# Optimization experiments

Measured on AMD Instinct MI355X. Metric: run time of the kernel, lower is better.

Reference implementation:

```python
import jax, jax.numpy as jnp
import numpy as np


def _ln(x, g, b, eps=1e-5):
    m = x.mean(-1, keepdims=True)
    v = ((x - m) ** 2).mean(-1, keepdims=True)
    return (x - m) / jnp.sqrt(v + eps) * g + b


def _conv(x, w, b, stride, pad, groups):
    # x: NCHW, w: OIHW (I = in_ch/groups)
    out = jax.lax.conv_general_dilated(
        x, w, (stride, stride), [(pad, pad), (pad, pad)],
        dimension_numbers=('NCHW', 'OIHW', 'NCHW'), feature_group_count=groups)
    return out + b[None, :, None, None]


def _gelu(x):
    return jax.nn.gelu(x, approximate=False)  # torch nn.GELU (exact erf)


def _forward(x, H, W, lpu_w, lpu_b, n1_g, n1_b, conv2d_w, conv2d_b, cn_g, cn_b,
             q_w, sr1_w, sr1_b, an1_g, an1_b, sr2_w, sr2_b, an2_g, an2_b,
             kv1_w, kv2_w, proj_w, proj_b, n2_g, n2_b,
             fc1_w, fc1_b, dw_w, dw_b, fc2_w, fc2_b):
    B, N, C = x.shape
    cd = C // 4          # conv_part_dim = 64
    ad = C - cd          # attn_part_dim = 192
    nh = 8
    hg = nh // 2         # heads per group
    hd = ad // nh        # head_dim = 24
    scale = hd ** -0.5
    # ---- LPU: depthwise 3x3 conv residual ----
    xi = x.transpose(0, 2, 1).reshape(B, C, H, W)
    xi = _conv(xi, lpu_w, lpu_b, 1, 1, C) + xi
    x = xi.reshape(B, C, N).transpose(0, 2, 1)
    # ---- Attention branch (pre-LN) ----
    y = _ln(x, n1_g, n1_b)
    cp, ap = y[..., :cd], y[..., cd:]
    # conv part: dense 3x3 conv (sr_ratio==8 -> kernel 3, pad 1), then LN+GELU in NLC
    cp = cp.reshape(B, H, W, cd).transpose(0, 3, 1, 2)
    cp = _conv(cp, conv2d_w, conv2d_b, 1, 1, 1).reshape(B, cd, N).transpose(0, 2, 1)
    cp = _gelu(_ln(cp, cn_g, cn_b))
    # attn part: dual spatial-reduction KV paths
    q = (ap @ q_w.T).reshape(B, N, nh, hd).transpose(0, 2, 1, 3)  # [B,nh,N,hd]
    x_ = ap.transpose(0, 2, 1).reshape(B, ad, H, W)
    x1 = _conv(x_, sr1_w, sr1_b, 8, 0, ad).reshape(B, ad, -1).transpose(0, 2, 1)  # [B,(H/8)(W/8),ad]
    x1 = _gelu(_ln(x1, an1_g, an1_b))
    x2 = _conv(x_, sr2_w, sr2_b, 4, 0, ad).reshape(B, ad, -1).transpose(0, 2, 1)  # [B,(H/4)(W/4),ad]
    x2 = _gelu(_ln(x2, an2_g, an2_b))
    kv1 = (x1 @ kv1_w.T).reshape(B, -1, 2, hg, hd).transpose(2, 0, 3, 1, 4)  # [2,B,hg,M1,hd]
    kv2 = (x2 @ kv2_w.T).reshape(B, -1, 2, hg, hd).transpose(2, 0, 3, 1, 4)

    def attn(qh, k, v):
        a = jax.nn.softmax(jnp.einsum('bhnd,bhmd->bhnm', qh, k) * scale, axis=-1)
        o = jnp.einsum('bhnm,bhmd->bhnd', a, v)
        return o.transpose(0, 2, 1, 3).reshape(B, N, -1)

    o1 = attn(q[:, :hg], kv1[0], kv1[1])
    o2 = attn(q[:, hg:], kv2[0], kv2[1])
    y = jnp.concatenate([o1, o2, cp], axis=-1) @ proj_w.T + proj_b
    x = x + y
    # ---- MLP with depthwise conv ----
    z = _ln(x, n2_g, n2_b) @ fc1_w.T + fc1_b
    hidc = z.shape[-1]
    z = z.transpose(0, 2, 1).reshape(B, hidc, H, W)
    z = _conv(z, dw_w, dw_b, 1, 1, hidc).reshape(B, hidc, N).transpose(0, 2, 1)
    z = _gelu(z) @ fc2_w.T + fc2_b
    return x + z


def setup_inputs() -> dict:
    key = jax.random.key(0)
    ks = jax.random.split(key, 16)
    B, H, W, C = 16, 56, 56, 256
    N = H * W
    cd, ad = C // 4, C * 3 // 4
    hid = 4 * C
    f = lambda i, shape, s=0.02: jax.random.normal(ks[i], shape, jnp.float32) * s
    return dict(
        x=jax.random.normal(ks[0], (B, N, C), jnp.float32),
        H=H, W=W,
        lpu_w=f(1, (C, 1, 3, 3), 0.1), lpu_b=jnp.zeros((C,), jnp.float32),
        n1_g=jnp.ones((C,), jnp.float32), n1_b=jnp.zeros((C,), jnp.float32),
        conv2d_w=f(2, (cd, cd, 3, 3), 0.05), conv2d_b=jnp.zeros((cd,), jnp.float32),
        cn_g=jnp.ones((cd,), jnp.float32), cn_b=jnp.zeros((cd,), jnp.float32),
        q_w=f(3, (ad, ad)),
        sr1_w=f(4, (ad, 1, 8, 8), 0.1), sr1_b=jnp.zeros((ad,), jnp.float32),
        an1_g=jnp.ones((ad,), jnp.float32), an1_b=jnp.zeros((ad,), jnp.float32),
        sr2_w=f(5, (ad, 1, 4, 4), 0.1), sr2_b=jnp.zeros((ad,), jnp.float32),
        an2_g=jnp.ones((ad,), jnp.float32), an2_b=jnp.zeros((ad,), jnp.float32),
        kv1_w=f(6, (ad, ad)), kv2_w=f(7, (ad, ad)),
        proj_w=f(8, (C, C)), proj_b=jnp.zeros((C,), jnp.float32),
        n2_g=jnp.ones((C,), jnp.float32), n2_b=jnp.zeros((C,), jnp.float32),
        fc1_w=f(9, (hid, C)), fc1_b=jnp.zeros((hid,), jnp.float32),
        dw_w=f(10, (hid, 1, 3, 3), 0.1), dw_b=jnp.zeros((hid,), jnp.float32),
        fc2_w=f(11, (C, hid)), fc2_b=jnp.zeros((C,), jnp.float32),
    )


def reference(x, H, W, lpu_w, lpu_b, n1_g, n1_b, conv2d_w, conv2d_b, cn_g, cn_b,
              q_w, sr1_w, sr1_b, an1_g, an1_b, sr2_w, sr2_b, an2_g, an2_b,
              kv1_w, kv2_w, proj_w, proj_b, n2_g, n2_b,
              fc1_w, fc1_b, dw_w, dw_b, fc2_w, fc2_b):
    return _forward(x, H, W, lpu_w, lpu_b, n1_g, n1_b, conv2d_w, conv2d_b, cn_g, cn_b,
                    q_w, sr1_w, sr1_b, an1_g, an1_b, sr2_w, sr2_b, an2_g, an2_b,
                    kv1_w, kv2_w, proj_w, proj_b, n2_g, n2_b,
                    fc1_w, fc1_b, dw_w, dw_b, fc2_w, fc2_b)
```

## Files before the change

### kernel.cpp

```cpp
#include <hip/hip_runtime.h>
#include <math.h>

#define BB   16
#define HH   56
#define WW   56
#define NN   (HH*WW)
#define CC   256
#define CD   64
#define AD   192
#define NH   8
#define HG   4
#define HD   24
#define HID  1024
#define M1   49
#define M2   196
#define BNR  (BB*NN)

typedef __attribute__((ext_vector_type(8))) short s8v;
typedef __attribute__((ext_vector_type(4))) short s4v;
typedef __attribute__((ext_vector_type(4))) float f4v;
typedef __attribute__((ext_vector_type(8))) _Float16 h8v;
typedef __attribute__((ext_vector_type(2))) _Float16 h2v;

__device__ __forceinline__ float gelu_f(float x) {
    float u = x * (1.0f + 0.044715f * x * x);
    float t = __expf(-1.5957691216f * u);
    return x * __builtin_amdgcn_rcpf(1.0f + t);
}
__device__ __forceinline__ ushort f2bf(float f) {
    union { float f; uint32_t u; } c; c.f = f;
    uint32_t u = c.u;
    return (ushort)((u + 0x7fffu + ((u >> 16) & 1u)) >> 16);
}
__device__ __forceinline__ float bf2f(ushort u) {
    union { uint32_t u; float f; } c; c.u = ((uint32_t)u) << 16;
    return c.f;
}
__device__ __forceinline__ ushort f2h(float f) {
    union { _Float16 h; ushort u; } c; c.h = (_Float16)f;
    return c.u;
}
__device__ __forceinline__ void load_lds16(const void* gsrc, void* ldst) {
    __builtin_amdgcn_global_load_lds(
        (const __attribute__((address_space(1))) void*)gsrc,
        (__attribute__((address_space(3))) void*)ldst, 16, 0, 0);
}
__device__ __forceinline__ int xcd_swz(int bid, int nwg) {
    int q = nwg >> 3, r = nwg & 7;
    int x = bid & 7, i = bid >> 3;
    return (x < r ? x * (q + 1) : r * (q + 1) + (x - r) * q) + i;
}

__global__ __launch_bounds__(256) void wprep_kernel(
        const float* __restrict__ qw, const float* __restrict__ k1,
        const float* __restrict__ k2, const float* __restrict__ pw,
        const float* __restrict__ f1, const float* __restrict__ f2,
        const float* __restrict__ cw, const float* __restrict__ lw,
        const float* __restrict__ dw,
        ushort* __restrict__ wq, ushort* __restrict__ wkv1,
        ushort* __restrict__ wkv2, ushort* __restrict__ wpr,
        ushort* __restrict__ wf1, ushort* __restrict__ wf2,
        ushort* __restrict__ wcp, float* __restrict__ lpwt,
        ushort* __restrict__ dwwth) {
    int i = blockIdx.x * 256 + threadIdx.x;
    if (i < 36864) { wq[i] = f2bf(qw[i]); return; } i -= 36864;
    if (i < 36864) { wkv1[i] = f2bf(k1[i]); return; } i -= 36864;
    if (i < 36864) { wkv2[i] = f2bf(k2[i]); return; } i -= 36864;
    if (i < 65536) { wpr[i] = f2bf(pw[i]); return; } i -= 65536;
    if (i < 262144) { wf1[i] = f2bf(f1[i]); return; } i -= 262144;
    if (i < 262144) { wf2[i] = f2h(f2[i]); return; } i -= 262144;
    if (i < 36864) {
        int co = i / 576, k = i - co * 576;
        int tap = k >> 6, ci = k & 63;
        wcp[i] = f2bf(cw[co * 576 + ci * 9 + tap]);
        return;
    } i -= 36864;
    if (i < 2304) { int c = i / 9, t = i - c * 9; lpwt[t * CC + c] = lw[i]; return; } i -= 2304;
    if (i < 9216) { int c = i / 9, t = i - c * 9; dwwth[t * HID + c] = f2h(dw[i]); }
}

__global__ __launch_bounds__(256) void lpu_kernel(const float* __restrict__ x,
        const float* __restrict__ wt, const float* __restrict__ bias,
        const float* __restrict__ n1g, const float* __restrict__ n1b,
        ushort* __restrict__ xbuf, ushort* __restrict__ ybuf) {
    int tid = threadIdx.x;
    int lane = tid & 63, wv = tid >> 6;
    int c = lane * 4;
    int grp = xcd_swz(blockIdx.x, NN / 16) * 4 + wv;
    int n0 = grp * 4;
    int h = n0 / WW, x0 = n0 - h * WW;
    int b = blockIdx.y;
    const float* xb = x + (size_t)b * NN * CC + c;
    float4 wreg[9];
#pragma unroll
    for (int t = 0; t < 9; ++t) wreg[t] = *(const float4*)(wt + t * CC + c);
    float4 bz = *(const float4*)(bias + c);
    float4 acc[4] = {bz, bz, bz, bz};
#pragma unroll
    for (int cx = 0; cx < 6; ++cx) {
        int wx = x0 + cx - 1;
        if ((unsigned)wx >= (unsigned)WW) continue;
#pragma unroll
        for (int ky = 0; ky < 3; ++ky) {
            int hy = h + ky - 1;
            if ((unsigned)hy >= (unsigned)HH) continue;
            float4 xv = *(const float4*)(xb + (size_t)(hy * WW + wx) * CC);
#pragma unroll
            for (int xo = 0; xo < 4; ++xo) {
                int kx = cx - xo;
                if (kx < 0 || kx > 2) continue;
                float4 wv4 = wreg[ky * 3 + kx];
                acc[xo].x = fmaf(xv.x, wv4.x, acc[xo].x);
                acc[xo].y = fmaf(xv.y, wv4.y, acc[xo].y);
                acc[xo].z = fmaf(xv.z, wv4.z, acc[xo].z);
                acc[xo].w = fmaf(xv.w, wv4.w, acc[xo].w);
            }
        }
    }
    float4 gv = *(const float4*)(n1g + c);
    float4 bv = *(const float4*)(n1b + c);
#pragma unroll
    for (int xo = 0; xo < 4; ++xo) {
        size_t o = ((size_t)b * NN + n0 + xo) * CC + c;
        float4 rv = *(const float4*)(x + o);
        float4 a = acc[xo];
        a.x += rv.x; a.y += rv.y; a.z += rv.z; a.w += rv.w;
        s4v xv4;
        xv4.x = (short)f2bf(a.x);
        xv4.y = (short)f2bf(a.y);
        xv4.z = (short)f2bf(a.z);
        xv4.w = (short)f2bf(a.w);
        *(s4v*)(xbuf + o) = xv4;
        float s = a.x + a.y + a.z + a.w;
        float sq = a.x * a.x + a.y * a.y + a.z * a.z + a.w * a.w;
#pragma unroll
        for (int off = 32; off >= 1; off >>= 1) {
            s += __shfl_xor(s, off, 64);
            sq += __shfl_xor(sq, off, 64);
        }
        float mean = s * (1.0f / 256.0f);
        float var = sq * (1.0f / 256.0f) - mean * mean;
        float rstd = rsqrtf(var + 1e-5f);
        s4v ov;
        ov.x = (short)f2bf((a.x - mean) * rstd * gv.x + bv.x);
        ov.y = (short)f2bf((a.y - mean) * rstd * gv.y + bv.y);
        ov.z = (short)f2bf((a.z - mean) * rstd * gv.z + bv.z);
        ov.w = (short)f2bf((a.w - mean) * rstd * gv.w + bv.w);
        *(s4v*)(ybuf + o) = ov;
    }
}

__global__ __launch_bounds__(256) void cpgemm_kernel(
        const ushort* __restrict__ y, const ushort* __restrict__ wt,
        const float* __restrict__ cb, const float* __restrict__ cng,
        const float* __restrict__ cnb, ushort* __restrict__ cat) {
    __shared__ __align__(16) ushort As[128 * 32];
    __shared__ __align__(16) ushort Ws[64 * 32];
    int tid = threadIdx.x;
    int wid = tid >> 6, lane = tid & 63;
    int rt = xcd_swz(blockIdx.x, BNR / 128) * 128;
    int r0 = tid >> 2, c0 = tid & 3;
    int r1 = r0 + 64;
    int tok0 = rt + r0, tok1 = rt + r1;
    int b0 = tok0 / NN, n0 = tok0 - b0 * NN, h0 = n0 / WW, w0 = n0 - h0 * WW;
    int b1 = tok1 / NN, n1 = tok1 - b1 * NN, h1 = n1 / WW, w1 = n1 - h1 * WW;
    const ushort* Wp = wt + (size_t)r0 * 576 + c0 * 8;
    int aw0 = (c0 ^ (r0 & 3)) << 3;
    f4v acc[2][4];
#pragma unroll
    for (int m = 0; m < 2; ++m)
#pragma unroll
        for (int n = 0; n < 4; ++n) acc[m][n] = (f4v)0.f;
    int lr = lane & 15, g4 = lane >> 4;
    int swz = (g4 ^ (lr & 3)) << 3;
    for (int kt = 0; kt < 576; kt += 32) {
        int tap = kt >> 6, ci0 = kt & 63;
        int t3 = tap / 3, dy = t3 - 1, dx = (tap - t3 * 3) - 1;
        s8v a0 = (s8v)0, a1 = (s8v)0;
        int hy0 = h0 + dy, wx0 = w0 + dx;
        if ((unsigned)hy0 < (unsigned)HH && (unsigned)wx0 < (unsigned)WW)
            a0 = *(const s8v*)(y + ((size_t)b0 * NN + hy0 * WW + wx0) * CC + ci0 + c0 * 8);
        int hy1 = h1 + dy, wx1 = w1 + dx;
        if ((unsigned)hy1 < (unsigned)HH && (unsigned)wx1 < (unsigned)WW)
            a1 = *(const s8v*)(y + ((size_t)b1 * NN + hy1 * WW + wx1) * CC + ci0 + c0 * 8);
        s8v wv = *(const s8v*)(Wp + kt);
        __syncthreads();
        *(s8v*)&As[r0 * 32 + aw0] = a0;
        *(s8v*)&As[r1 * 32 + aw0] = a1;
        *(s8v*)&Ws[r0 * 32 + aw0] = wv;
        __syncthreads();
        s8v af[2], bf[4];
#pragma unroll
        for (int m = 0; m < 2; ++m)
            af[m] = *(const s8v*)&As[(wid * 32 + m * 16 + lr) * 32 + swz];
#pragma unroll
        for (int n = 0; n < 4; ++n)
            bf[n] = *(const s8v*)&Ws[(n * 16 + lr) * 32 + swz];
#pragma unroll
        for (int m = 0; m < 2; ++m)
#pragma unroll
            for (int n = 0; n < 4; ++n)
                acc[m][n] = __builtin_amdgcn_mfma_f32_16x16x32_bf16(af[m], bf[n], acc[m][n], 0, 0, 0);
    }
    float gv[4], bv[4], cbv[4];
#pragma unroll
    for (int n = 0; n < 4; ++n) {
        int gc = n * 16 + lr;
        cbv[n] = cb[gc];
        gv[n] = cng[gc];
        bv[n] = cnb[gc];
    }
#pragma unroll
    for (int m = 0; m < 2; ++m)
#pragma unroll
        for (int r = 0; r < 4; ++r) {
            float s = 0.f, sq = 0.f;
#pragma unroll
            for (int n = 0; n < 4; ++n) {
                float v = acc[m][n][r] + cbv[n];
                acc[m][n][r] = v;
                s += v; sq += v * v;
            }
#pragma unroll
            for (int off = 1; off < 16; off <<= 1) {
                s += __shfl_xor(s, off, 64);
                sq += __shfl_xor(sq, off, 64);
            }
            float mean = s * (1.0f / 64.0f);
            float var = sq * (1.0f / 64.0f) - mean * mean;
            float rstd = rsqrtf(var + 1e-5f);
            int row = rt + wid * 32 + m * 16 + g4 * 4 + r;
            ushort* op = cat + (size_t)row * CC + 192;
#pragma unroll
            for (int n = 0; n < 4; ++n) {
                float v = (acc[m][n][r] - mean) * rstd * gv[n] + bv[n];
                op[n * 16 + lr] = f2bf(gelu_f(v));
            }
        }
}

template <int KS, int OW>
__device__ __forceinline__ void sr_body(const ushort* __restrict__ yap,
        const float* __restrict__ w, const float* __restrict__ bias,
        const float* __restrict__ g, const float* __restrict__ bt,
        ushort* __restrict__ out, int m, int b) {
    int ch = threadIdx.x;
    int oh = m / OW, ow = m - oh * OW;
    const ushort* yb = yap + (size_t)b * NN * CC;
    float acc = bias[ch];
#pragma unroll
    for (int ky = 0; ky < KS; ++ky)
#pragma unroll
        for (int kx = 0; kx < KS; ++kx)
            acc = fmaf(bf2f(yb[(size_t)((oh * KS + ky) * WW + ow * KS + kx) * CC + ch]),
                       w[ch * KS * KS + ky * KS + kx], acc);
    __shared__ float red[2][3];
    float s = acc, sq = acc * acc;
#pragma unroll
    for (int off = 32; off >= 1; off >>= 1) {
        s += __shfl_xor(s, off, 64);
        sq += __shfl_xor(sq, off, 64);
    }
    int wv = threadIdx.x >> 6, lane = threadIdx.x & 63;
    if (lane == 0) { red[0][wv] = s; red[1][wv] = sq; }
    __syncthreads();
    s = red[0][0] + red[0][1] + red[0][2];
    sq = red[1][0] + red[1][1] + red[1][2];
    float mean = s * (1.0f / 192.0f);
    float var = sq * (1.0f / 192.0f) - mean * mean;
    float rstd = rsqrtf(var + 1e-5f);
    float v = (acc - mean) * rstd * g[ch] + bt[ch];
    out[((size_t)b * (OW * OW) + m) * AD + ch] = f2bf(gelu_f(v));
}

__global__ __launch_bounds__(192) void sr_both(const ushort* __restrict__ yap,
        const float* __restrict__ w1, const float* __restrict__ b1,
        const float* __restrict__ g1, const float* __restrict__ t1,
        ushort* __restrict__ o1,
        const float* __restrict__ w2, const float* __restrict__ b2,
        const float* __restrict__ g2, const float* __restrict__ t2,
        ushort* __restrict__ o2) {
    int b = blockIdx.y;
    if (blockIdx.x < M2) sr_body<4, 14>(yap, w2, b2, g2, t2, o2, blockIdx.x, b);
    else                 sr_body<8, 7>(yap, w1, b1, g1, t1, o1, blockIdx.x - M2, b);
}

template <int MODE, int F16>
__device__ __forceinline__ void gemm_body(
        const ushort* __restrict__ A, int lda,
        const ushort* __restrict__ W, int K, int O,
        const float* __restrict__ bias,
        const ushort* __restrict__ res, int ldr,
        void* __restrict__ Cout, int ldc, int R,
        int gx, int nwg, int bid) {
    __shared__ __align__(16) ushort As[2 * 256 * 32];
    __shared__ __align__(16) ushort Ws[2 * 128 * 32];
    int tid = threadIdx.x;
    int w8 = tid >> 6, lane = tid & 63;
    int wr = w8 >> 1, wc = w8 & 1;
    int swzb = xcd_swz(bid, nwg);
    int rt = (swzb / gx) * 256, ot = (swzb % gx) * 128;
    int r0 = tid >> 2, cslot = tid & 3;
    int csrc = (cslot ^ (r0 & 3)) * 8;
    const ushort* Ap0 = A + (size_t)min(rt + r0, R - 1) * lda + csrc;
    const ushort* Ap1 = A + (size_t)min(rt + r0 + 128, R - 1) * lda + csrc;
    const ushort* Wp0 = W + (size_t)min(ot + r0, O - 1) * K + csrc;
    char* lA0 = (char*)As + w8 * 1024;
    char* lA1 = (char*)As + 8192 + w8 * 1024;
    char* lW0 = (char*)Ws + w8 * 1024;
    f4v acc[4][4];
#pragma unroll
    for (int m = 0; m < 4; ++m)
#pragma unroll
        for (int n = 0; n < 4; ++n) acc[m][n] = (f4v)0.f;
    int lr = lane & 15;
    int swz = ((lane >> 4) ^ (lr & 3)) << 3;
    load_lds16(Ap0, lA0);
    load_lds16(Ap1, lA1);
    load_lds16(Wp0, lW0);
    __syncthreads();
    int cur = 0;
    for (int kt = 0; kt < K; kt += 32) {
        if (kt + 32 < K) {
            int pa = (cur ^ 1) * 16384, pw = (cur ^ 1) * 8192;
            load_lds16(Ap0 + kt + 32, lA0 + pa);
            load_lds16(Ap1 + kt + 32, lA1 + pa);
            load_lds16(Wp0 + kt + 32, lW0 + pw);
        }
        const ushort* Ab = As + cur * 8192;
        const ushort* Wb = Ws + cur * 4096;
        s8v af[4], bf[4];
#pragma unroll
        for (int m = 0; m < 4; ++m)
            af[m] = *(const s8v*)&Ab[(wr * 64 + m * 16 + lr) * 32 + swz];
#pragma unroll
        for (int n = 0; n < 4; ++n)
            bf[n] = *(const s8v*)&Wb[(wc * 64 + n * 16 + lr) * 32 + swz];
#pragma unroll
        for (int m = 0; m < 4; ++m)
#pragma unroll
            for (int n = 0; n < 4; ++n) {
                if (F16) {
                    h8v ah = *(const h8v*)&af[m];
                    h8v bh = *(const h8v*)&bf[n];
                    acc[m][n] = __builtin_amdgcn_mfma_f32_16x16x32_f16(ah, bh, acc[m][n], 0, 0, 0);
                } else {
                    acc[m][n] = __builtin_amdgcn_mfma_f32_16x16x32_bf16(af[m], bf[n], acc[m][n], 0, 0, 0);
                }
            }
        __syncthreads();
        cur ^= 1;
    }
#pragma unroll
    for (int m = 0; m < 4; ++m)
#pragma unroll
        for (int n = 0; n < 4; ++n) {
            int gr = rt + wr * 64 + m * 16 + (lane >> 4) * 4;
            int gc = ot + wc * 64 + n * 16 + (lane & 15);
            if (gc >= O) continue;
#pragma unroll
            for (int r = 0; r < 4; ++r) {
                int row = gr + r;
                if (row >= R) continue;
                float v = acc[m][n][r];
                if (MODE & 1) v += bias[gc];
                if (MODE & 2) v += bf2f(res[(size_t)row * ldr + gc]);
                if (MODE & 4)      ((ushort*)Cout)[(size_t)row * ldc + gc] = f2bf(v);
                else if (MODE & 8) ((ushort*)Cout)[(size_t)row * ldc + gc] = f2h(v);
                else               ((float*)Cout)[(size_t)row * ldc + gc] = v;
            }
        }
}

template <int MODE, int F16 = 0>
__global__ __launch_bounds__(512) void gemm_mfma(
        const ushort* __restrict__ A, int lda,
        const ushort* __restrict__ W, int K, int O,
        const float* __restrict__ bias,
        const ushort* __restrict__ res, int ldr,
        void* __restrict__ Cout, int ldc, int R) {
    gemm_body<MODE, F16>(A, lda, W, K, O, bias, res, ldr, Cout, ldc, R,
                         gridDim.x, gridDim.x * gridDim.y,
                         blockIdx.y * gridDim.x + blockIdx.x);
}

__global__ __launch_bounds__(512) void kv_both(
        const ushort* __restrict__ x1g, const ushort* __restrict__ wkv1,
        ushort* __restrict__ kv1b,
        const ushort* __restrict__ x2g, const ushort* __restrict__ wkv2,
        ushort* __restrict__ kv2b) {
    int bid = blockIdx.y * 2 + blockIdx.x;
    if (blockIdx.z == 0) {
        if (blockIdx.y >= 4) return;
        gemm_body<4, 0>(x1g, AD, wkv1, AD, AD, nullptr, nullptr, 0,
                        kv1b, AD, BB * M1, 2, 8, bid);
    } else {
        gemm_body<4, 0>(x2g, AD, wkv2, AD, AD, nullptr, nullptr, 0,
                        kv2b, AD, BB * M2, 2, 26, bid);
    }
}

template <int MODE, int F16 = 0>
__global__ __launch_bounds__(1024) void gemm_8ph(
        const ushort* __restrict__ A, int lda,
        const ushort* __restrict__ W, int K, int O,
        const float* __restrict__ bias,
        const ushort* __restrict__ res, int ldr,
        void* __restrict__ Cout, int ldc, int R) {
    __shared__ __align__(16) ushort Al[2 * 256 * 64];
    __shared__ __align__(16) ushort Wl[2 * 256 * 64];
    int tid = threadIdx.x;
    int w16 = tid >> 6, lane = tid & 63;
    int wr = w16 >> 2, wc = w16 & 3;
    int nwg = gridDim.x * gridDim.y;
    int swzb = xcd_swz(blockIdx.y * gridDim.x + blockIdx.x, nwg);
    int rt = (swzb / gridDim.x) * 256, ot = (swzb % gridDim.x) * 256;
    int lr = lane & 15, g4 = lane >> 4;
    int swz = (g4 ^ (lr & 3)) << 3;
    int ar0 = tid >> 2, sp0 = tid & 3;
    int cs0 = ((sp0 ^ (ar0 & 3)) << 3);
    const ushort* Ap0 = A + (size_t)(rt + ar0) * lda + cs0;
    const ushort* Wp0 = W + (size_t)(ot + ar0) * K + cs0;
    int d0 = w16 * 1024;
    f4v acc[4][4];
#pragma unroll
    for (int m = 0; m < 4; ++m)
#pragma unroll
        for (int n = 0; n < 4; ++n)
            acc[m][n] = (f4v)((MODE & 1) ? bias[ot + wc * 64 + n * 16 + lr] : 0.0f);
    auto STAGE = [&](int s) {
        int t = s >> 1, hf = s & 1;
        int boff = (t & 1) * 32768 + hf * 16384;
        int kc = t * 64 + hf * 32;
        load_lds16(Ap0 + kc, (char*)Al + boff + d0);
        load_lds16(Wp0 + kc, (char*)Wl + boff + d0);
    };
    int nS = K >> 5;
    STAGE(0); STAGE(1); STAGE(2);
    for (int s = 0; s < nS; ++s) {
        if (s < nS - 2)       asm volatile("s_waitcnt vmcnt(4)" ::: "memory");
        else if (s == nS - 2) asm volatile("s_waitcnt vmcnt(2)" ::: "memory");
        else                  asm volatile("s_waitcnt vmcnt(0)" ::: "memory");
        __builtin_amdgcn_s_barrier();
        __builtin_amdgcn_sched_barrier(0);
        if (s + 3 < nS) STAGE(s + 3);
        int uoff = ((s >> 1) & 1) * 16384 + (s & 1) * 8192;
        const ushort* Ab = Al + uoff;
        const ushort* Wb = Wl + uoff;
        s8v af[4], bf[4];
#pragma unroll
        for (int m = 0; m < 4; ++m)
            af[m] = *(const s8v*)&Ab[(wr * 64 + m * 16 + lr) * 32 + swz];
#pragma unroll
        for (int n = 0; n < 4; ++n)
            bf[n] = *(const s8v*)&Wb[(wc * 64 + n * 16 + lr) * 32 + swz];
        __builtin_amdgcn_s_setprio(1);
#pragma unroll
        for (int m = 0; m < 4; ++m)
#pragma unroll
            for (int n = 0; n < 4; ++n) {
                if (F16) {
                    h8v ah = *(const h8v*)&af[m];
                    h8v bh = *(const h8v*)&bf[n];
                    acc[m][n] = __builtin_amdgcn_mfma_f32_16x16x32_f16(ah, bh, acc[m][n], 0, 0, 0);
                } else {
                    acc[m][n] = __builtin_amdgcn_mfma_f32_16x16x32_bf16(af[m], bf[n], acc[m][n], 0, 0, 0);
                }
            }
        __builtin_amdgcn_s_setprio(0);
    }
#pragma unroll
    for (int m = 0; m < 4; ++m) {
        int gr = rt + wr * 64 + m * 16 + g4 * 4;
#pragma unroll
        for (int n = 0; n < 4; ++n) {
            int gc = ot + wc * 64 + n * 16 + lr;
#pragma unroll
            for (int r = 0; r < 4; ++r) {
                int row = gr + r;
                float v = acc[m][n][r];
                if (MODE & 2) v += bf2f(res[(size_t)row * ldr + gc]);
                if (MODE & 4)      ((ushort*)Cout)[(size_t)row * ldc + gc] = f2bf(v);
                else if (MODE & 8) ((ushort*)Cout)[(size_t)row * ldc + gc] = f2h(v);
                else               ((float*)Cout)[(size_t)row * ldc + gc] = v;
            }
        }
    }
}

__global__ __launch_bounds__(512) void projln_kernel(
        const ushort* __restrict__ A, const ushort* __restrict__ W,
        const float* __restrict__ bias,
        const float* __restrict__ n2g, const float* __restrict__ n2b,
        ushort* __restrict__ xbuf, ushort* __restrict__ ybuf) {
    __shared__ __align__(16) ushort As[128 * 32];
    __shared__ __align__(16) ushort Ws[256 * 32];
    int tid = threadIdx.x;
    int w8 = tid >> 6, lane = tid & 63;
    int rt = xcd_swz(blockIdx.x, BNR / 128) * 128;
    int r0 = tid >> 2, cslot = tid & 3;
    int csrc = (cslot ^ (r0 & 3)) * 8;
    const ushort* Ap0 = A + (size_t)(rt + r0) * CC + csrc;
    const ushort* Wp0 = W + (size_t)r0 * CC + csrc;
    const ushort* Wp1 = W + (size_t)(r0 + 128) * CC + csrc;
    char* lA0 = (char*)As + w8 * 1024;
    char* lW0 = (char*)Ws + w8 * 1024;
    char* lW1 = (char*)Ws + 8192 + w8 * 1024;
    int lr = lane & 15, g4 = lane >> 4;
    int swz = (g4 ^ (lr & 3)) << 3;
    f4v acc[16];
#pragma unroll
    for (int n = 0; n < 16; ++n) acc[n] = (f4v)(bias[n * 16 + lr]);
    for (int kt = 0; kt < CC; kt += 32) {
        __syncthreads();
        load_lds16(Ap0 + kt, lA0);
        load_lds16(Wp0 + kt, lW0);
        load_lds16(Wp1 + kt, lW1);
        __syncthreads();
        s8v af = *(const s8v*)&As[(w8 * 16 + lr) * 32 + swz];
#pragma unroll
        for (int n = 0; n < 16; ++n) {
            s8v bf = *(const s8v*)&Ws[(n * 16 + lr) * 32 + swz];
            acc[n] = __builtin_amdgcn_mfma_f32_16x16x32_bf16(af, bf, acc[n], 0, 0, 0);
        }
    }
#pragma unroll
    for (int r = 0; r < 4; ++r) {
        int row = rt + w8 * 16 + g4 * 4 + r;
        ushort* xr = xbuf + (size_t)row * CC;
        ushort* yr = ybuf + (size_t)row * CC;
        float s = 0.f, sq = 0.f;
#pragma unroll
        for (int n = 0; n < 16; ++n) {
            float v = acc[n][r] + bf2f(xr[n * 16 + lr]);
            acc[n][r] = v;
            s += v; sq += v * v;
        }
#pragma unroll
        for (int off = 1; off < 16; off <<= 1) {
            s += __shfl_xor(s, off, 64);
            sq += __shfl_xor(sq, off, 64);
        }
        float mean = s * (1.0f / 256.0f);
        float var = sq * (1.0f / 256.0f) - mean * mean;
        float rstd = rsqrtf(var + 1e-5f);
#pragma unroll
        for (int n = 0; n < 16; ++n) {
            int col = n * 16 + lr;
            float v = acc[n][r];
            xr[col] = f2bf(v);
            yr[col] = f2bf((v - mean) * rstd * n2g[col] + n2b[col]);
        }
    }
}

template <int M, int MP>
__device__ __forceinline__ void attn_body(const ushort* __restrict__ q,
        const ushort* __restrict__ kvb, ushort* __restrict__ cat,
        ushort* Kl, ushort* VT, int g, int h, int b) {
    constexpr int NT = MP / 16;
    constexpr int NCH = MP / 32;
    int tid = threadIdx.x;
    for (int i = tid; i < MP * 4; i += 256) ((s8v*)Kl)[i] = (s8v)0;
    for (int i = tid; i < MP * 4; i += 256) ((s8v*)VT)[i] = (s8v)0;
    __syncthreads();
    for (int u = tid; u < M * 3; u += 256) {
        int m = u / 3, d0 = u - m * 3;
        s8v kv8 = *(const s8v*)(kvb + ((size_t)b * M + m) * AD + g * HD + d0 * 8);
        *(s8v*)&Kl[m * 32 + ((d0 ^ (m & 3)) << 3)] = kv8;
    }
    for (int u = tid; u < M * 3; u += 256) {
        int m = u / 3, d0 = u - m * 3;
        s8v vv = *(const s8v*)(kvb + ((size_t)b * M + m) * AD + 96 + g * HD + d0 * 8);
        int c = m >> 5, mm = m & 31;
        int gg = (mm >> 2) & 3;
        int t = (mm & 3) + ((mm & 16) >> 2);
#pragma unroll
        for (int j = 0; j < 8; ++j) {
            int d = d0 * 8 + j;
            VT[d * MP + ((c * 4 + (gg ^ (d & 3))) << 3) + t] = (ushort)vv[j];
        }
    }
    __syncthreads();
    int w = tid >> 6, lane = tid & 63;
    int ln = lane & 15, g4 = lane >> 4;
    int swz = (g4 ^ (ln & 3)) << 3;
    const float scale = 0.20412414523193154f;
    for (int nt = 0; nt < 4; ++nt) {
        int nbase = blockIdx.x * 256 + nt * 64;
        if (nbase >= NN) break;
        int n0 = nbase + w * 16 + ln;
        s8v qf = (s8v)0;
        if (g4 < 3) qf = *(const s8v*)(q + ((size_t)b * NN + n0) * AD + h * HD + g4 * 8);
        f4v sa[NT];
#pragma unroll
        for (int t = 0; t < NT; ++t) sa[t] = (f4v)0.f;
#pragma unroll
        for (int t = 0; t < NT; ++t) {
            s8v kf = *(const s8v*)&Kl[(t * 16 + ln) * 32 + swz];
            sa[t] = __builtin_amdgcn_mfma_f32_16x16x32_bf16(kf, qf, sa[t], 0, 0, 0);
        }
        float mx = -3.0e38f;
#pragma unroll
        for (int t = 0; t < NT; ++t)
#pragma unroll
            for (int r = 0; r < 4; ++r) {
                int m = t * 16 + g4 * 4 + r;
                float v = (m < M) ? sa[t][r] * scale : -3.0e38f;
                sa[t][r] = v;
                mx = fmaxf(mx, v);
            }
        mx = fmaxf(mx, __shfl_xor(mx, 16, 64));
        mx = fmaxf(mx, __shfl_xor(mx, 32, 64));
        float sum = 0.f;
#pragma unroll
        for (int t = 0; t < NT; ++t)
#pragma unroll
            for (int r = 0; r < 4; ++r) {
                float p = __expf(sa[t][r] - mx);
                sa[t][r] = p;
                sum += p;
            }
        sum += __shfl_xor(sum, 16, 64);
        sum += __shfl_xor(sum, 32, 64);
        float inv = 1.0f / sum;
        f4v oa[2] = {(f4v)0.f, (f4v)0.f};
#pragma unroll
        for (int c = 0; c < NCH; ++c) {
            s8v pb;
#pragma unroll
            for (int t = 0; t < 4; ++t) {
                pb[t]     = (short)f2bf(sa[c * 2][t]);
                pb[4 + t] = (short)f2bf(sa[c * 2 + 1][t]);
            }
#pragma unroll
            for (int dt = 0; dt < 2; ++dt) {
                s8v vf = *(const s8v*)&VT[(dt * 16 + ln) * MP + c * 32 + swz];
                oa[dt] = __builtin_amdgcn_mfma_f32_16x16x32_bf16(vf, pb, oa[dt], 0, 0, 0);
            }
        }
        ushort* op = cat + ((size_t)b * NN + n0) * CC + h * HD;
        s4v o0;
#pragma unroll
        for (int r = 0; r < 4; ++r) o0[r] = (short)f2bf(oa[0][r] * inv);
        *(s4v*)(op + g4 * 4) = o0;
        if (g4 < 2) {
            s4v o1;
#pragma unroll
            for (int r = 0; r < 4; ++r) o1[r] = (short)f2bf(oa[1][r] * inv);
            *(s4v*)(op + 16 + g4 * 4) = o1;
        }
    }
}

__global__ __launch_bounds__(256) void attn_both(const ushort* __restrict__ q,
        const ushort* __restrict__ kv1b, const ushort* __restrict__ kv2b,
        ushort* __restrict__ cat) {
    __shared__ __align__(16) ushort Kl[224 * 32];
    __shared__ __align__(16) ushort VT[32 * 224];
    int hy = blockIdx.y, b = blockIdx.z;
    if (hy < HG) attn_body<M1, 64>(q, kv1b, cat, Kl, VT, hy, hy, b);
    else         attn_body<M2, 224>(q, kv2b, cat, Kl, VT, hy - HG, hy, b);
}

__global__ __launch_bounds__(256) void dwconv_kernel(const ushort* __restrict__ z1,
        const ushort* __restrict__ wt, const float* __restrict__ bias,
        ushort* __restrict__ z2) {
    int bid = xcd_swz(blockIdx.x, HH * 7);
    int h = bid / 7, bx = bid - h * 7;
    int b = blockIdx.y;
    int c = (threadIdx.x & 127) * 8;
    int x0 = bx * 8 + (threadIdx.x >> 7) * 4;
    const ushort* zrow = z1 + ((size_t)b * NN + h * WW) * HID + c;
    h2v wreg[9][4];
#pragma unroll
    for (int t = 0; t < 9; ++t) {
        s8v w8 = *(const s8v*)(wt + t * HID + c);
        const h2v* wp = (const h2v*)&w8;
#pragma unroll
        for (int p = 0; p < 4; ++p) wreg[t][p] = wp[p];
    }
    h2v acc[4][4];
    {
        float4 b0 = *(const float4*)(bias + c);
        float4 b1 = *(const float4*)(bias + c + 4);
        h2v bz[4];
        bz[0][0] = (_Float16)b0.x; bz[0][1] = (_Float16)b0.y;
        bz[1][0] = (_Float16)b0.z; bz[1][1] = (_Float16)b0.w;
        bz[2][0] = (_Float16)b1.x; bz[2][1] = (_Float16)b1.y;
        bz[3][0] = (_Float16)b1.z; bz[3][1] = (_Float16)b1.w;
#pragma unroll
        for (int xo = 0; xo < 4; ++xo)
#pragma unroll
            for (int p = 0; p < 4; ++p) acc[xo][p] = bz[p];
    }
#pragma unroll
    for (int cx = 0; cx < 6; ++cx) {
        int wx = x0 + cx - 1;
        if ((unsigned)wx >= (unsigned)WW) continue;
#pragma unroll
        for (int ky = 0; ky < 3; ++ky) {
            int hy = h + ky - 1;
            if ((unsigned)hy >= (unsigned)HH) continue;
            s8v v = *(const s8v*)(zrow + ((size_t)(ky - 1) * WW + wx) * HID);
            const h2v* v2 = (const h2v*)&v;
#pragma unroll
            for (int xo = 0; xo < 4; ++xo) {
                int kx = cx - xo;
                if (kx < 0 || kx > 2) continue;
#pragma unroll
                for (int p = 0; p < 4; ++p)
                    acc[xo][p] = v2[p] * wreg[ky * 3 + kx][p] + acc[xo][p];
            }
        }
    }
    ushort* zo = z2 + ((size_t)b * NN + h * WW + x0) * HID + c;
#pragma unroll
    for (int xo = 0; xo < 4; ++xo) {
        s8v o;
#pragma unroll
        for (int p = 0; p < 4; ++p) {
            o[p * 2]     = (short)f2h(gelu_f((float)acc[xo][p][0]));
            o[p * 2 + 1] = (short)f2h(gelu_f((float)acc[xo][p][1]));
        }
        *(s8v*)(zo + (size_t)xo * HID) = o;
    }
}

extern "C" void kernel_launch(void* const* d_in, const int* in_sizes, int n_in,
                              void* d_out, int out_size, void* d_ws, size_t ws_size,
                              hipStream_t stream) {
    const float* x      = (const float*)d_in[0];
    const float* lpu_w  = (const float*)d_in[3];
    const float* lpu_b  = (const float*)d_in[4];
    const float* n1_g   = (const float*)d_in[5];
    const float* n1_b   = (const float*)d_in[6];
    const float* c2_w   = (const float*)d_in[7];
    const float* c2_b   = (const float*)d_in[8];
    const float* cn_g   = (const float*)d_in[9];
    const float* cn_b   = (const float*)d_in[10];
    const float* q_w    = (const float*)d_in[11];
    const float* sr1_w  = (const float*)d_in[12];
    const float* sr1_b  = (const float*)d_in[13];
    const float* an1_g  = (const float*)d_in[14];
    const float* an1_b  = (const float*)d_in[15];
    const float* sr2_w  = (const float*)d_in[16];
    const float* sr2_b  = (const float*)d_in[17];
    const float* an2_g  = (const float*)d_in[18];
    const float* an2_b  = (const float*)d_in[19];
    const float* kv1_w  = (const float*)d_in[20];
    const float* kv2_w  = (const float*)d_in[21];
    const float* proj_w = (const float*)d_in[22];
    const float* proj_b = (const float*)d_in[23];
    const float* n2_g   = (const float*)d_in[24];
    const float* n2_b   = (const float*)d_in[25];
    const float* fc1_w  = (const float*)d_in[26];
    const float* fc1_b  = (const float*)d_in[27];
    const float* dw_w   = (const float*)d_in[28];
    const float* dw_b   = (const float*)d_in[29];
    const float* fc2_w  = (const float*)d_in[30];
    const float* fc2_b  = (const float*)d_in[31];
    float* out = (float*)d_out;

    char* ws = (char*)d_ws;
    size_t off = 0;
    auto allocB = [&](size_t bytes) {
        char* p = ws + off;
        off += ((bytes + 255) & ~(size_t)255);
        return p;
    };
    ushort* xbuf = (ushort*)allocB((size_t)BNR * CC * 2);
    ushort* ybuf = (ushort*)allocB((size_t)BNR * CC * 2);
    ushort* wq   = (ushort*)allocB((size_t)AD * AD * 2);
    ushort* wkv1 = (ushort*)allocB((size_t)AD * AD * 2);
    ushort* wkv2 = (ushort*)allocB((size_t)AD * AD * 2);
    ushort* wpr  = (ushort*)allocB((size_t)CC * CC * 2);
    ushort* wf1  = (ushort*)allocB((size_t)HID * CC * 2);
    ushort* wf2  = (ushort*)allocB((size_t)CC * HID * 2);
    ushort* wcp  = (ushort*)allocB((size_t)64 * 576 * 2);
    float*  lpwt = (float*)allocB((size_t)9 * CC * 4);
    ushort* dwwt = (ushort*)allocB((size_t)9 * HID * 2);
    size_t zmark = off;
    ushort* cat  = (ushort*)allocB((size_t)BNR * CC * 2);
    ushort* qbuf = (ushort*)allocB((size_t)BNR * AD * 2);
    ushort* x1g  = (ushort*)allocB((size_t)BB * M1 * AD * 2);
    ushort* x2g  = (ushort*)allocB((size_t)BB * M2 * AD * 2);
    ushort* kv1b = (ushort*)allocB((size_t)BB * M1 * AD * 2);
    ushort* kv2b = (ushort*)allocB((size_t)BB * M2 * AD * 2);

    int CB2 = 1;
    for (int cb = 16; cb >= 1; cb >>= 1) {
        if (zmark + 2 * (size_t)cb * NN * HID * 2 <= ws_size) { CB2 = cb; break; }
    }

    dim3 b256(256), b512(512), b1024(1024);
    wprep_kernel<<<dim3(2925), b256, 0, stream>>>(
        q_w, kv1_w, kv2_w, proj_w, fc1_w, fc2_w, c2_w, lpu_w, dw_w,
        wq, wkv1, wkv2, wpr, wf1, wf2, wcp, lpwt, dwwt);
    lpu_kernel<<<dim3(NN / 16, BB), b256, 0, stream>>>(x, lpwt, lpu_b, n1_g, n1_b, xbuf, ybuf);
    cpgemm_kernel<<<dim3(BNR / 128), b256, 0, stream>>>(ybuf, wcp, c2_b, cn_g, cn_b, cat);
    gemm_mfma<4><<<dim3(2, BNR / 256), b512, 0, stream>>>(
        ybuf + CD, CC, wq, AD, AD, nullptr, nullptr, 0, qbuf, AD, BNR);
    sr_both<<<dim3(M1 + M2, BB), dim3(192), 0, stream>>>(ybuf + CD,
        sr1_w, sr1_b, an1_g, an1_b, x1g, sr2_w, sr2_b, an2_g, an2_b, x2g);
    kv_both<<<dim3(2, 13, 2), b512, 0, stream>>>(x1g, wkv1, kv1b, x2g, wkv2, kv2b);
    attn_both<<<dim3((NN + 255) / 256, NH, BB), b256, 0, stream>>>(qbuf, kv1b, kv2b, cat);
    projln_kernel<<<dim3(BNR / 128), b512, 0, stream>>>(
        cat, wpr, proj_b, n2_g, n2_b, xbuf, ybuf);
    ushort* z1 = (ushort*)(ws + zmark);
    ushort* z2 = z1 + (size_t)CB2 * NN * HID;
    for (int c0 = 0; c0 < BB; c0 += CB2) {
        size_t tokoff = (size_t)c0 * NN;
        int Rr = CB2 * NN;
        gemm_8ph<9><<<dim3(HID / 256, Rr / 256), b1024, 0, stream>>>(
            ybuf + tokoff * CC, CC, wf1, CC, HID, fc1_b, nullptr, 0, z1, HID, Rr);
        dwconv_kernel<<<dim3(HH * 7, CB2), b256, 0, stream>>>(z1, dwwt, dw_b, z2);
        gemm_8ph<3, 1><<<dim3(CC / 256, Rr / 256), b1024, 0, stream>>>(
            z2, HID, wf2, HID, CC, fc2_b, xbuf + tokoff * CC, CC, out + tokoff * CC, CC, Rr);
    }
}
```

Measured before the change: 339.5 us.

## Merge Q projection into KV GEMM launch and fold conv-part GEMM into attention

Combines the Q projection GEMM with the two KV projection GEMMs in a single three-slice launch. The dense 3x3 conv-part GEMM becomes a device function run by an extra slice of blocks in the attention kernel, reusing its shared memory. The goal is fewer kernel launches and letting independent work run alongside the attention blocks. The cost is grid imbalance, many idle early-return blocks, and a conv GEMM that is now tied to the attention kernel's 256-thread block shape and shared-memory footprint.

```diff
diff --git a/kernel.cpp b/kernel.cpp
--- a/kernel.cpp
+++ b/kernel.cpp
@@ -150,15 +150,14 @@
     }
 }
 
-__global__ __launch_bounds__(256) void cpgemm_kernel(
+__device__ __forceinline__ void cpgemm_body(
         const ushort* __restrict__ y, const ushort* __restrict__ wt,
         const float* __restrict__ cb, const float* __restrict__ cng,
-        const float* __restrict__ cnb, ushort* __restrict__ cat) {
-    __shared__ __align__(16) ushort As[128 * 32];
-    __shared__ __align__(16) ushort Ws[64 * 32];
+        const float* __restrict__ cnb, ushort* __restrict__ cat,
+        ushort* As , ushort* Ws , int tile) {
     int tid = threadIdx.x;
     int wid = tid >> 6, lane = tid & 63;
-    int rt = xcd_swz(blockIdx.x, BNR / 128) * 128;
+    int rt = xcd_swz(tile, BNR / 128) * 128;
     int r0 = tid >> 2, c0 = tid & 3;
     int r1 = r0 + 64;
     int tok0 = rt + r0, tok1 = rt + r1;
@@ -372,29 +371,23 @@
         }
 }
 
-template <int MODE, int F16 = 0>
-__global__ __launch_bounds__(512) void gemm_mfma(
-        const ushort* __restrict__ A, int lda,
-        const ushort* __restrict__ W, int K, int O,
-        const float* __restrict__ bias,
-        const ushort* __restrict__ res, int ldr,
-        void* __restrict__ Cout, int ldc, int R) {
-    gemm_body<MODE, F16>(A, lda, W, K, O, bias, res, ldr, Cout, ldc, R,
-                         gridDim.x, gridDim.x * gridDim.y,
-                         blockIdx.y * gridDim.x + blockIdx.x);
-}
-
-__global__ __launch_bounds__(512) void kv_both(
+__global__ __launch_bounds__(512) void kvq_all(
+        const ushort* __restrict__ yap, const ushort* __restrict__ wq,
+        ushort* __restrict__ qbuf,
         const ushort* __restrict__ x1g, const ushort* __restrict__ wkv1,
         ushort* __restrict__ kv1b,
         const ushort* __restrict__ x2g, const ushort* __restrict__ wkv2,
         ushort* __restrict__ kv2b) {
     int bid = blockIdx.y * 2 + blockIdx.x;
     if (blockIdx.z == 0) {
+        gemm_body<4, 0>(yap, CC, wq, AD, AD, nullptr, nullptr, 0,
+                        qbuf, AD, BNR, 2, 392, bid);
+    } else if (blockIdx.z == 1) {
         if (blockIdx.y >= 4) return;
         gemm_body<4, 0>(x1g, AD, wkv1, AD, AD, nullptr, nullptr, 0,
                         kv1b, AD, BB * M1, 2, 8, bid);
     } else {
+        if (blockIdx.y >= 13) return;
         gemm_body<4, 0>(x2g, AD, wkv2, AD, AD, nullptr, nullptr, 0,
                         kv2b, AD, BB * M2, 2, 26, bid);
     }
@@ -655,12 +648,21 @@
 
 __global__ __launch_bounds__(256) void attn_both(const ushort* __restrict__ q,
         const ushort* __restrict__ kv1b, const ushort* __restrict__ kv2b,
-        ushort* __restrict__ cat) {
+        ushort* __restrict__ cat,
+        const ushort* __restrict__ ybuf, const ushort* __restrict__ wcp,
+        const float* __restrict__ cb, const float* __restrict__ cng,
+        const float* __restrict__ cnb) {
     __shared__ __align__(16) ushort Kl[224 * 32];
     __shared__ __align__(16) ushort VT[32 * 224];
     int hy = blockIdx.y, b = blockIdx.z;
-    if (hy < HG) attn_body<M1, 64>(q, kv1b, cat, Kl, VT, hy, hy, b);
-    else         attn_body<M2, 224>(q, kv2b, cat, Kl, VT, hy - HG, hy, b);
+    if (hy < HG)      attn_body<M1, 64>(q, kv1b, cat, Kl, VT, hy, hy, b);
+    else if (hy < NH) attn_body<M2, 224>(q, kv2b, cat, Kl, VT, hy - HG, hy, b);
+    else {
+        int id = blockIdx.x + 13 * blockIdx.z;
+        for (int t = id * 2; t < id * 2 + 2; ++t)
+            if (t < BNR / 128)
+                cpgemm_body(ybuf, wcp, cb, cng, cnb, cat, Kl, VT, t);
+    }
 }
 
 __global__ __launch_bounds__(256) void dwconv_kernel(const ushort* __restrict__ z1,
@@ -798,13 +800,12 @@
         q_w, kv1_w, kv2_w, proj_w, fc1_w, fc2_w, c2_w, lpu_w, dw_w,
         wq, wkv1, wkv2, wpr, wf1, wf2, wcp, lpwt, dwwt);
     lpu_kernel<<<dim3(NN / 16, BB), b256, 0, stream>>>(x, lpwt, lpu_b, n1_g, n1_b, xbuf, ybuf);
-    cpgemm_kernel<<<dim3(BNR / 128), b256, 0, stream>>>(ybuf, wcp, c2_b, cn_g, cn_b, cat);
-    gemm_mfma<4><<<dim3(2, BNR / 256), b512, 0, stream>>>(
-        ybuf + CD, CC, wq, AD, AD, nullptr, nullptr, 0, qbuf, AD, BNR);
     sr_both<<<dim3(M1 + M2, BB), dim3(192), 0, stream>>>(ybuf + CD,
         sr1_w, sr1_b, an1_g, an1_b, x1g, sr2_w, sr2_b, an2_g, an2_b, x2g);
-    kv_both<<<dim3(2, 13, 2), b512, 0, stream>>>(x1g, wkv1, kv1b, x2g, wkv2, kv2b);
-    attn_both<<<dim3((NN + 255) / 256, NH, BB), b256, 0, stream>>>(qbuf, kv1b, kv2b, cat);
+    kvq_all<<<dim3(2, 196, 3), b512, 0, stream>>>(
+        ybuf + CD, wq, qbuf, x1g, wkv1, kv1b, x2g, wkv2, kv2b);
+    attn_both<<<dim3((NN + 255) / 256, NH + 1, BB), b256, 0, stream>>>(
+        qbuf, kv1b, kv2b, cat, ybuf, wcp, c2_b, cn_g, cn_b);
     projln_kernel<<<dim3(BNR / 128), b512, 0, stream>>>(
         cat, wpr, proj_b, n2_g, n2_b, xbuf, ybuf);
     ushort* z1 = (ushort*)(ws + zmark);
```

Measured after the change: 332.4 us, median of 2. 1.02x faster.
